# Kernel optimization log

Measured on AMD Instinct MI355X. Metric: run time of the kernel, lower is better.

## Reference

```python
import jax, jax.numpy as jnp
import numpy as np

B, N, P_FEATS = 8, 4096, 3
WIDTH, HEADS, LAYERS, N_LAT = 768, 12, 8, 256
NUM_FREQS = 8
D_HEAD = WIDTH // HEADS
SCALE = 1.0 / np.sqrt(np.sqrt(D_HEAD))  # applied to q and k separately
IN_DIM = 3 * (1 + 2 * NUM_FREQS) + P_FEATS  # 54
EPS = 1e-5


def fourier_embed(pc):
    # pc: [B,N,3] -> [B,N,51] (include_input + sin/cos at freqs 2^0..2^7)
    freqs = (2.0 ** jnp.arange(NUM_FREQS)).astype(pc.dtype)
    ang = pc[..., None] * freqs  # [B,N,3,F]
    ang = ang.reshape(*pc.shape[:-1], 3 * NUM_FREQS)
    return jnp.concatenate([pc, jnp.sin(ang), jnp.cos(ang)], axis=-1)


def layernorm(x, s, b):
    mu = jnp.mean(x, axis=-1, keepdims=True)
    var = jnp.mean(jnp.square(x - mu), axis=-1, keepdims=True)
    return (x - mu) * jax.lax.rsqrt(var + EPS) * s + b


def mh_attn(q, k, v):
    # q: [B,T,H,C], k/v: [B,S,H,C]
    w = jnp.einsum('bthc,bshc->bhts', q * SCALE, k * SCALE)
    w = jax.nn.softmax(w.astype(jnp.float32), axis=-1).astype(q.dtype)
    out = jnp.einsum('bhts,bshc->bthc', w, v)
    return out.reshape(*q.shape[:2], -1)


def setup_inputs() -> dict:
    key = jax.random.key(0)
    ks = iter(jax.random.split(key, 64))
    rn = lambda shape, std=0.02: jax.random.normal(next(ks), shape, jnp.float32) * std
    inp = {
        'pc': jax.random.normal(next(ks), (B, N, 3), jnp.float32),
        'feats': jax.random.uniform(next(ks), (B, N, P_FEATS), jnp.float32),
        'query': rn((N_LAT, WIDTH)),
        'in_W': rn((WIDTH, IN_DIM)), 'in_b': jnp.zeros((WIDTH,)),
        'ca_qkv_W': rn((3 * WIDTH, WIDTH)), 'ca_qkv_b': jnp.zeros((3 * WIDTH,)),
        'ca_proj_W': rn((WIDTH, WIDTH)), 'ca_proj_b': jnp.zeros((WIDTH,)),
        'ln1_s': jnp.ones((LAYERS, WIDTH)), 'ln1_b': jnp.zeros((LAYERS, WIDTH)),
        'qkv_W': rn((LAYERS, 3 * WIDTH, WIDTH)), 'qkv_b': jnp.zeros((LAYERS, 3 * WIDTH)),
        'proj_W': rn((LAYERS, WIDTH, WIDTH)), 'proj_b': jnp.zeros((LAYERS, WIDTH)),
        'ln2_s': jnp.ones((LAYERS, WIDTH)), 'ln2_b': jnp.zeros((LAYERS, WIDTH)),
        'fc_W': rn((LAYERS, 4 * WIDTH, WIDTH)), 'fc_b': jnp.zeros((LAYERS, 4 * WIDTH)),
        'fc2_W': rn((LAYERS, WIDTH, 4 * WIDTH)), 'fc2_b': jnp.zeros((LAYERS, WIDTH)),
    }
    return inp


def _forward(pc, feats, query, in_W, in_b, ca_qkv_W, ca_qkv_b, ca_proj_W, ca_proj_b,
             ln1_s, ln1_b, qkv_W, qkv_b, proj_W, proj_b, ln2_s, ln2_b,
             fc_W, fc_b, fc2_W, fc2_b):
    bs = pc.shape[0]
    data = jnp.concatenate([fourier_embed(pc), feats], axis=-1)  # [B,N,54]
    data = data @ in_W.T + in_b  # [B,N,W]
    q_lat = jnp.broadcast_to(query[None], (bs, N_LAT, WIDTH))

    # --- cross attention (no residual, matching source) ---
    q = (q_lat @ ca_qkv_W.T + ca_qkv_b)[..., :WIDTH]
    kv = data @ ca_qkv_W.T + ca_qkv_b
    k, v = kv[..., WIDTH:2 * WIDTH], kv[..., 2 * WIDTH:]
    q = q.reshape(bs, N_LAT, HEADS, D_HEAD)
    k = k.reshape(bs, N, HEADS, D_HEAD)
    v = v.reshape(bs, N, HEADS, D_HEAD)
    latents = mh_attn(q, k, v) @ ca_proj_W.T + ca_proj_b  # [B,L,W]

    # --- self-attention transformer stack via scan ---
    def block(x, p):
        (l1s, l1b, qW, qb, pW, pb, l2s, l2b, fW, fb, f2W, f2b) = p
        h = layernorm(x, l1s, l1b)
        qkv = (h @ qW.T + qb).reshape(bs, N_LAT, HEADS, 3 * D_HEAD)
        qh, kh, vh = jnp.split(qkv, 3, axis=-1)
        x = x + mh_attn(qh, kh, vh) @ pW.T + pb
        h = layernorm(x, l2s, l2b)
        h = jax.nn.gelu(h @ fW.T + fb, approximate=False) @ f2W.T + f2b
        return x + h, None

    params = (ln1_s, ln1_b, qkv_W, qkv_b, proj_W, proj_b, ln2_s, ln2_b, fc_W, fc_b, fc2_W, fc2_b)
    latents, _ = jax.lax.scan(block, latents, params)
    return latents, pc


def reference(pc, feats, query, in_W, in_b, ca_qkv_W, ca_qkv_b, ca_proj_W, ca_proj_b,
              ln1_s, ln1_b, qkv_W, qkv_b, proj_W, proj_b, ln2_s, ln2_b,
              fc_W, fc_b, fc2_W, fc2_b):
    return _forward(pc, feats, query, in_W, in_b, ca_qkv_W, ca_qkv_b, ca_proj_W, ca_proj_b,
                    ln1_s, ln1_b, qkv_W, qkv_b, proj_W, proj_b, ln2_s, ln2_b,
                    fc_W, fc_b, fc2_W, fc2_b)
```

## Files before the change

### kernel.cpp

```cpp
#include <hip/hip_runtime.h>
#include <stdint.h>

typedef unsigned short u16;
typedef __bf16 bf16x8 __attribute__((ext_vector_type(8)));
typedef float f32x4 __attribute__((ext_vector_type(4)));

#define DEVINL __device__ __forceinline__

DEVINL u16 f2bf(float f) {
  union { float f; unsigned u; } c; c.f = f;
  unsigned u = c.u + 0x7FFFu + ((c.u >> 16) & 1u);
  return (u16)(u >> 16);
}

DEVINL float bf2f(u16 v) {
  union { unsigned u; float f; } c; c.u = (unsigned)v << 16;
  return c.f;
}

DEVINL unsigned pk2bf(float a, float b) {
#if __has_builtin(__builtin_amdgcn_cvt_pk_bf16_f32)
  auto r = __builtin_amdgcn_cvt_pk_bf16_f32(a, b);
  unsigned u;
  __builtin_memcpy(&u, &r, 4);
  return u;
#else
  return (unsigned)f2bf(a) | ((unsigned)f2bf(b) << 16);
#endif
}

DEVINL void gl2lds16(const void* g, void* l) {
  __builtin_amdgcn_global_load_lds(
      (const __attribute__((address_space(1))) unsigned int*)g,
      (__attribute__((address_space(3))) unsigned int*)l, 16, 0, 0);
}

template <int N> DEVINL void waitvm() {
  asm volatile("s_waitcnt vmcnt(%0)" ::"n"(N) : "memory");
}
DEVINL void bar() {
  asm volatile("" ::: "memory");
  __builtin_amdgcn_s_barrier();
  asm volatile("" ::: "memory");
}

__global__ __launch_bounds__(256) void cvt4_kernel(
    const float* __restrict__ s0, u16* __restrict__ d0, int n0,
    const float* __restrict__ s1, u16* __restrict__ d1, int n1,
    const float* __restrict__ s2, u16* __restrict__ d2, int n2,
    const float* __restrict__ s3, u16* __restrict__ d3, int n3) {
  int i = blockIdx.x * 256 + threadIdx.x;
  const float* s; u16* d;
  if (i < n0) { s = s0; d = d0; }
  else {
    i -= n0;
    if (i < n1) { s = s1; d = d1; }
    else {
      i -= n1;
      if (i < n2) { s = s2; d = d2; }
      else {
        i -= n2;
        if (i >= n3) return;
        s = s3; d = d3;
      }
    }
  }
  float4 v = ((const float4*)s)[i];
  ((uint2*)d)[i] = make_uint2(pk2bf(v.x, v.y), pk2bf(v.z, v.w));
}

__global__ __launch_bounds__(256) void pad_inwT_kernel(const float* __restrict__ src,
                                                       u16* __restrict__ dst) {
  int t = blockIdx.x * 256 + threadIdx.x;
  if (t >= 64 * 768) return;
  int j = t / 768, o = t - j * 768;
  dst[t] = (j < 54) ? f2bf(src[o * 54 + j]) : (u16)0;
}

__global__ __launch_bounds__(256) void bprime_kernel(const float* __restrict__ caW,
                                                     const float* __restrict__ caB,
                                                     const float* __restrict__ inb,
                                                     float* __restrict__ bp) {
  int w = threadIdx.x >> 6, lane = threadIdx.x & 63;
  int m = blockIdx.x * 4 + w;
  const float* row = caW + (size_t)(768 + m) * 768;
  float s = 0.f;
#pragma unroll
  for (int k = 0; k < 12; k++) s += row[lane + k * 64] * inb[lane + k * 64];
#pragma unroll
  for (int msk = 32; msk >= 1; msk >>= 1) s += __shfl_xor(s, msk, 64);
  if (lane == 0) bp[m] = s + caB[768 + m];
}

__global__ __launch_bounds__(256) void embed_kernel(const float* __restrict__ pc,
                                                    const float* __restrict__ feats,
                                                    u16* __restrict__ emb) {
  int t = blockIdx.x * 256 + threadIdx.x;
  int p = t >> 6, c = t & 63;
  float v = 0.f;
  if (c < 3) {
    v = pc[p * 3 + c];
  } else if (c < 27) {
    int i = c - 3;
    float f = (float)(1 << (i & 7));
    v = sinf(pc[p * 3 + (i >> 3)] * f);
  } else if (c < 51) {
    int i = c - 27;
    float f = (float)(1 << (i & 7));
    v = cosf(pc[p * 3 + (i >> 3)] * f);
  } else if (c < 54) {
    v = feats[p * 3 + (c - 51)];
  }
  emb[t] = f2bf(v);
}

template <int TM, int TN, int WR, int WC, int MODE>
__global__ __launch_bounds__(256) void gemm_t(
    const u16* __restrict__ A, const u16* __restrict__ Bw,
    const float* __restrict__ bias, const float* __restrict__ resid,
    float* __restrict__ outF, u16* __restrict__ outB,
    int M, int N, int Nout, int K, int gelu,
    u16* __restrict__ vt, int vy, int skvt, int bsh) {
  constexpr int IM = TM / WR / 16;
  constexpr int IN = TN / WC / 16;
  __shared__ u16 As[TM * 32];
  __shared__ u16 Bs[TN * 32];
  const int tid = threadIdx.x;
  const int lane = tid & 63, w = tid >> 6;
  const int l15 = lane & 15, quad = lane >> 4;
  const int mblk = blockIdx.x * TM, nblk = blockIdx.y * TN;
  const int wm = (w % WR) * (TM / WR);
  const int wn = (w / WR) * (TN / WC);

  f32x4 acc[IM][IN];
#pragma unroll
  for (int i = 0; i < IM; i++)
#pragma unroll
    for (int j = 0; j < IN; j++) acc[i][j] = f32x4{0.f, 0.f, 0.f, 0.f};

  bool tv = false;
  if (MODE == 1) tv = ((int)blockIdx.y >= vy);
  if (MODE == 2) tv = ((int)(blockIdx.y % 3) == 2);

  if (!tv) {
    for (int k0 = 0; k0 < K; k0 += 32) {
#pragma unroll
      for (int s = tid; s < TM * 4; s += 256) {
        int row = s >> 2, c8 = (s & 3) << 3;
        gl2lds16(A + (size_t)(mblk + row) * K + (k0 + c8), &As[s * 8]);
      }
#pragma unroll
      for (int s = tid; s < TN * 4; s += 256) {
        int row = s >> 2, c8 = (s & 3) << 3;
        gl2lds16(Bw + (size_t)(nblk + row) * K + (k0 + c8), &Bs[s * 8]);
      }
      __syncthreads();
      bf16x8 af[IM], bfr[IN];
#pragma unroll
      for (int i = 0; i < IM; i++)
        af[i] = *(const bf16x8*)&As[(wm + i * 16 + l15) * 32 + quad * 8];
#pragma unroll
      for (int j = 0; j < IN; j++)
        bfr[j] = *(const bf16x8*)&Bs[(wn + j * 16 + l15) * 32 + quad * 8];
#pragma unroll
      for (int i = 0; i < IM; i++)
#pragma unroll
        for (int j = 0; j < IN; j++)
          acc[i][j] = __builtin_amdgcn_mfma_f32_16x16x32_bf16(bfr[j], af[i], acc[i][j], 0, 0, 0);
      __syncthreads();
    }
#pragma unroll
    for (int i = 0; i < IM; i++) {
      int m = mblk + wm + i * 16 + l15;
#pragma unroll
      for (int j = 0; j < IN; j++) {
        int n0 = nblk + wn + j * 16 + quad * 4;
        float4 bv = bias ? *(const float4*)&bias[n0] : make_float4(0.f, 0.f, 0.f, 0.f);
        float v0 = acc[i][j][0] + bv.x;
        float v1 = acc[i][j][1] + bv.y;
        float v2 = acc[i][j][2] + bv.z;
        float v3 = acc[i][j][3] + bv.w;
        if (gelu) {
          v0 = 0.5f * v0 * (1.0f + erff(v0 * 0.70710678118f));
          v1 = 0.5f * v1 * (1.0f + erff(v1 * 0.70710678118f));
          v2 = 0.5f * v2 * (1.0f + erff(v2 * 0.70710678118f));
          v3 = 0.5f * v3 * (1.0f + erff(v3 * 0.70710678118f));
        }
        size_t idx = (size_t)m * Nout + n0;
        if (resid) {
          float4 rv = *(const float4*)&resid[idx];
          v0 += rv.x; v1 += rv.y; v2 += rv.z; v3 += rv.w;
        }
        if (outF) {
          float4 ov = {v0, v1, v2, v3};
          *(float4*)&outF[idx] = ov;
        }
        if (outB) {
          *(uint2*)&outB[idx] = make_uint2(pk2bf(v0, v1), pk2bf(v2, v3));
        }
      }
    }
  } else {
    for (int k0 = 0; k0 < K; k0 += 32) {
#pragma unroll
      for (int s = tid; s < TM * 4; s += 256) {
        int row = s >> 2, c8 = (s & 3) << 3;
        gl2lds16(A + (size_t)(mblk + row) * K + (k0 + c8), &As[s * 8]);
      }
#pragma unroll
      for (int s = tid; s < TN * 4; s += 256) {
        int row = s >> 2, c8 = (s & 3) << 3;
        gl2lds16(Bw + (size_t)(nblk + row) * K + (k0 + c8), &Bs[s * 8]);
      }
      __syncthreads();
      bf16x8 af[IM], bfr[IN];
#pragma unroll
      for (int i = 0; i < IM; i++)
        af[i] = *(const bf16x8*)&As[(wm + i * 16 + l15) * 32 + quad * 8];
#pragma unroll
      for (int j = 0; j < IN; j++)
        bfr[j] = *(const bf16x8*)&Bs[(wn + j * 16 + l15) * 32 + quad * 8];
#pragma unroll
      for (int i = 0; i < IM; i++)
#pragma unroll
        for (int j = 0; j < IN; j++)
          acc[i][j] = __builtin_amdgcn_mfma_f32_16x16x32_bf16(af[i], bfr[j], acc[i][j], 0, 0, 0);
      __syncthreads();
    }
    int msk = (1 << bsh) - 1;
#pragma unroll
    for (int j = 0; j < IN; j++) {
      int n = nblk + wn + j * 16 + l15;
      float bv = bias ? bias[n] : 0.f;
#pragma unroll
      for (int i = 0; i < IM; i++) {
        int m0 = mblk + wm + i * 16 + quad * 4;
        int b = m0 >> bsh;
        int s0 = m0 & msk;
        float v0 = acc[i][j][0] + bv;
        float v1 = acc[i][j][1] + bv;
        float v2 = acc[i][j][2] + bv;
        float v3 = acc[i][j][3] + bv;
        size_t vrow;
        if (MODE == 2) {
          int h = blockIdx.y / 3;
          vrow = (size_t)(b * 12 + h) * 64 + (wn + j * 16 + l15);
        } else {
          vrow = (size_t)b * 768 + (n - vy * TN);
        }
        size_t addr = vrow * skvt + s0;
        *(uint2*)&vt[addr] = make_uint2(pk2bf(v0, v1), pk2bf(v2, v3));
      }
    }
  }
}

template <int TM, int TN, int WR, int WC>
__global__ __launch_bounds__(256) void gemmsk_t(
    const u16* __restrict__ A, const u16* __restrict__ Bw,
    float* __restrict__ P, int M, int N, int K, int kchunk) {
  constexpr int IM = TM / WR / 16;
  constexpr int IN = TN / WC / 16;
  __shared__ u16 As[TM * 32];
  __shared__ u16 Bs[TN * 32];
  const int tid = threadIdx.x;
  const int lane = tid & 63, w = tid >> 6;
  const int l15 = lane & 15, quad = lane >> 4;
  const int mblk = blockIdx.x * TM, nblk = blockIdx.y * TN;
  const int wm = (w % WR) * (TM / WR);
  const int wn = (w / WR) * (TN / WC);
  const int kbeg = blockIdx.z * kchunk;
  const int kend = kbeg + kchunk;

  f32x4 acc[IM][IN];
#pragma unroll
  for (int i = 0; i < IM; i++)
#pragma unroll
    for (int j = 0; j < IN; j++) acc[i][j] = f32x4{0.f, 0.f, 0.f, 0.f};

  for (int k0 = kbeg; k0 < kend; k0 += 32) {
#pragma unroll
    for (int s = tid; s < TM * 4; s += 256) {
      int row = s >> 2, c8 = (s & 3) << 3;
      gl2lds16(A + (size_t)(mblk + row) * K + (k0 + c8), &As[s * 8]);
    }
#pragma unroll
    for (int s = tid; s < TN * 4; s += 256) {
      int row = s >> 2, c8 = (s & 3) << 3;
      gl2lds16(Bw + (size_t)(nblk + row) * K + (k0 + c8), &Bs[s * 8]);
    }
    __syncthreads();
    bf16x8 af[IM], bfr[IN];
#pragma unroll
    for (int i = 0; i < IM; i++)
      af[i] = *(const bf16x8*)&As[(wm + i * 16 + l15) * 32 + quad * 8];
#pragma unroll
    for (int j = 0; j < IN; j++)
      bfr[j] = *(const bf16x8*)&Bs[(wn + j * 16 + l15) * 32 + quad * 8];
#pragma unroll
    for (int i = 0; i < IM; i++)
#pragma unroll
      for (int j = 0; j < IN; j++)
        acc[i][j] = __builtin_amdgcn_mfma_f32_16x16x32_bf16(bfr[j], af[i], acc[i][j], 0, 0, 0);
    __syncthreads();
  }

  float* Pz = P + (size_t)blockIdx.z * M * N;
#pragma unroll
  for (int i = 0; i < IM; i++) {
    int m = mblk + wm + i * 16 + l15;
#pragma unroll
    for (int j = 0; j < IN; j++) {
      int n0 = nblk + wn + j * 16 + quad * 4;
      float4 ov = {acc[i][j][0], acc[i][j][1], acc[i][j][2], acc[i][j][3]};
      *(float4*)&Pz[(size_t)m * N + n0] = ov;
    }
  }
}

__global__ __launch_bounds__(256) void skred_kernel(
    const float* __restrict__ P, int nsk, int MN4, int N,
    const float* __restrict__ bias, const float* __restrict__ resid,
    float* __restrict__ outF, u16* __restrict__ outB) {
  int i = blockIdx.x * 256 + threadIdx.x;
  if (i >= MN4) return;
  float4 s = ((const float4*)P)[i];
  for (int z = 1; z < nsk; z++) {
    float4 t = ((const float4*)P)[(size_t)z * MN4 + i];
    s.x += t.x; s.y += t.y; s.z += t.z; s.w += t.w;
  }
  if (bias) {
    int n0 = (i * 4) % N;
    float4 b = *(const float4*)&bias[n0];
    s.x += b.x; s.y += b.y; s.z += b.z; s.w += b.w;
  }
  if (resid) {
    float4 r = ((const float4*)resid)[i];
    s.x += r.x; s.y += r.y; s.z += r.z; s.w += r.w;
  }
  if (outF) ((float4*)outF)[i] = s;
  if (outB) ((uint2*)outB)[i] = make_uint2(pk2bf(s.x, s.y), pk2bf(s.z, s.w));
}

__global__ __launch_bounds__(256) void flash_kernel(
    const u16* __restrict__ Q, long qb, int qrs, int qhs,
    const u16* __restrict__ Kp, long kb, int krs, int khs,
    const u16* __restrict__ Vt, u16* __restrict__ Out,
    u16* __restrict__ Part, float* __restrict__ Ml,
    int Skv, int nsplit, int kvlen, int nbh, float scale2) {
  __shared__ u16 Qs[64 * 64];
  __shared__ u16 Ks[2][64 * 64];
  __shared__ u16 Vs[2][64 * 64];
  __shared__ u16 Ps[64 * 72];

  const int tid = threadIdx.x;
  const int lane = tid & 63, w = tid >> 6;
  const int l15 = lane & 15, quad = lane >> 4;

  int bid = blockIdx.x;
  int grp = nbh * nsplit;
  int qt = bid / grp;
  int rem = bid - qt * grp;
  int bh = rem / nsplit;
  int split = rem - bh * nsplit;
  int h = bh % 12, b = bh / 12;

  const u16* Qbase = Q + (size_t)b * qb + (size_t)(qt * 64) * qrs + h * qhs;
  const u16* Kbase = Kp + (size_t)b * kb + (size_t)h * khs;
  const u16* Vbase = Vt + ((size_t)(b * 12 + h) * 64) * Skv;

  int kt0 = split * kvlen;

#pragma unroll
  for (int p = 0; p < 2; ++p) {
    int slot = tid + p * 256;
    int row = slot >> 3, c = slot & 7;
    int cg = (c - row) & 7;
    gl2lds16(Qbase + (size_t)row * qrs + cg * 8, &Qs[slot * 8]);
    gl2lds16(Kbase + (size_t)(kt0 + row) * krs + cg * 8, &Ks[0][slot * 8]);
    gl2lds16(Vbase + (size_t)row * Skv + kt0 + cg * 8, &Vs[0][slot * 8]);
  }
  __syncthreads();

  bf16x8 qa[2];
#pragma unroll
  for (int kk = 0; kk < 2; kk++)
    qa[kk] = *(const bf16x8*)&Qs[(w * 16 + l15) * 64 + ((kk * 4 + quad + l15) & 7) * 8];

  f32x4 zero = {0.f, 0.f, 0.f, 0.f};
  f32x4 O[4];
#pragma unroll
  for (int d = 0; d < 4; d++) O[d] = zero;
  float m_i = -1e30f, l_i = 0.f;

  int cur = 0;
  for (int kt = kt0; kt < kt0 + kvlen; kt += 64) {
    bool hasnext = (kt + 64 < kt0 + kvlen);
    if (hasnext) {
#pragma unroll
      for (int p = 0; p < 2; ++p) {
        int slot = tid + p * 256;
        int row = slot >> 3, c = slot & 7;
        int cg = (c - row) & 7;
        gl2lds16(Kbase + (size_t)(kt + 64 + row) * krs + cg * 8, &Ks[cur ^ 1][slot * 8]);
        gl2lds16(Vbase + (size_t)row * Skv + (kt + 64) + cg * 8, &Vs[cur ^ 1][slot * 8]);
      }
      waitvm<4>();
    } else {
      waitvm<0>();
    }
    bar();

    f32x4 St[4];
#pragma unroll
    for (int j = 0; j < 4; j++) St[j] = zero;
#pragma unroll
    for (int kk = 0; kk < 2; kk++) {
#pragma unroll
      for (int j = 0; j < 4; j++) {
        bf16x8 kf = *(const bf16x8*)&Ks[cur][(j * 16 + l15) * 64 + ((kk * 4 + quad + l15) & 7) * 8];
        St[j] = __builtin_amdgcn_mfma_f32_16x16x32_bf16(kf, qa[kk], St[j], 0, 0, 0);
      }
    }

    float mx = St[0][0];
#pragma unroll
    for (int j = 0; j < 4; j++)
#pragma unroll
      for (int r = 0; r < 4; r++) mx = fmaxf(mx, St[j][r]);
    mx = fmaxf(mx, __shfl_xor(mx, 16, 64));
    mx = fmaxf(mx, __shfl_xor(mx, 32, 64));
    mx *= scale2;

    bool skip = __all(mx <= m_i + 8.f);
    float al = 1.f;
    if (!skip) {
      float mnew = fmaxf(m_i, mx);
      al = __expf(m_i - mnew);
      m_i = mnew;
    }
    float mref = m_i;
    float sum = 0.f;
#pragma unroll
    for (int j = 0; j < 4; j++) {
      float p0 = __expf(fmaf(St[j][0], scale2, -mref));
      float p1 = __expf(fmaf(St[j][1], scale2, -mref));
      float p2 = __expf(fmaf(St[j][2], scale2, -mref));
      float p3 = __expf(fmaf(St[j][3], scale2, -mref));
      sum += (p0 + p1) + (p2 + p3);
      *(uint2*)&Ps[(w * 16 + l15) * 72 + j * 16 + quad * 4] =
          make_uint2(pk2bf(p0, p1), pk2bf(p2, p3));
    }
    sum += __shfl_xor(sum, 16, 64);
    sum += __shfl_xor(sum, 32, 64);

    if (skip) {
      l_i += sum;
    } else {
      l_i = l_i * al + sum;
      float a0 = __shfl(al, quad * 20 + 0, 64);
      float a1 = __shfl(al, quad * 20 + 1, 64);
      float a2 = __shfl(al, quad * 20 + 2, 64);
      float a3 = __shfl(al, quad * 20 + 3, 64);
#pragma unroll
      for (int d = 0; d < 4; d++) {
        O[d][0] *= a0; O[d][1] *= a1; O[d][2] *= a2; O[d][3] *= a3;
      }
    }
    __asm__ __volatile__("s_waitcnt lgkmcnt(0)" ::: "memory");
#pragma unroll
    for (int kk = 0; kk < 2; kk++) {
      bf16x8 pa = *(const bf16x8*)&Ps[(w * 16 + l15) * 72 + kk * 32 + quad * 8];
#pragma unroll
      for (int d = 0; d < 4; d++) {
        bf16x8 vf = *(const bf16x8*)&Vs[cur][(d * 16 + l15) * 64 + ((kk * 4 + quad + l15) & 7) * 8];
        O[d] = __builtin_amdgcn_mfma_f32_16x16x32_bf16(pa, vf, O[d], 0, 0, 0);
      }
    }
    bar();
    cur ^= 1;
  }

  float l0 = __shfl(l_i, quad * 20 + 0, 64);
  float l1 = __shfl(l_i, quad * 20 + 1, 64);
  float l2 = __shfl(l_i, quad * 20 + 2, 64);
  float l3 = __shfl(l_i, quad * 20 + 3, 64);

  if (nsplit == 1) {
    float inv0 = 1.f / l0, inv1 = 1.f / l1, inv2 = 1.f / l2, inv3 = 1.f / l3;
    u16* Ob = Out + ((size_t)(b * 256 + qt * 64 + w * 16 + quad * 4)) * 768 + h * 64 + l15;
#pragma unroll
    for (int d = 0; d < 4; d++) {
      Ob[(size_t)0 * 768 + d * 16] = f2bf(O[d][0] * inv0);
      Ob[(size_t)1 * 768 + d * 16] = f2bf(O[d][1] * inv1);
      Ob[(size_t)2 * 768 + d * 16] = f2bf(O[d][2] * inv2);
      Ob[(size_t)3 * 768 + d * 16] = f2bf(O[d][3] * inv3);
    }
  } else {
    float m0 = __shfl(m_i, quad * 20 + 0, 64);
    float m1 = __shfl(m_i, quad * 20 + 1, 64);
    float m2 = __shfl(m_i, quad * 20 + 2, 64);
    float m3 = __shfl(m_i, quad * 20 + 3, 64);
    u16* Pb = Part + ((size_t)(bh * 4 + qt) * nsplit + split) * 4096;
    int rowb = w * 16 + quad * 4;
#pragma unroll
    for (int d = 0; d < 4; d++) {
      Pb[(rowb + 0) * 64 + d * 16 + l15] = f2bf(O[d][0]);
      Pb[(rowb + 1) * 64 + d * 16 + l15] = f2bf(O[d][1]);
      Pb[(rowb + 2) * 64 + d * 16 + l15] = f2bf(O[d][2]);
      Pb[(rowb + 3) * 64 + d * 16 + l15] = f2bf(O[d][3]);
    }
    if (l15 == 0) {
      float* MlB = Ml + ((size_t)(bh * 4 + qt) * nsplit + split) * 128;
      MlB[rowb + 0] = m0; MlB[rowb + 1] = m1; MlB[rowb + 2] = m2; MlB[rowb + 3] = m3;
      MlB[64 + rowb + 0] = l0; MlB[64 + rowb + 1] = l1;
      MlB[64 + rowb + 2] = l2; MlB[64 + rowb + 3] = l3;
    }
  }
}

__global__ __launch_bounds__(256) void freduce_kernel(
    const u16* __restrict__ Part, const float* __restrict__ Ml,
    u16* __restrict__ Out, int nsplit) {
  int bid = blockIdx.x;
  int qt = bid & 3, bh = bid >> 2;
  int h = bh % 12, b = bh / 12;
  int tid = threadIdx.x;
  int r = tid >> 2, dc = tid & 3;
  const float* mlb = Ml + (size_t)(bh * 4 + qt) * nsplit * 128;
  float M = -1e30f;
  for (int s = 0; s < nsplit; s++) M = fmaxf(M, mlb[s * 128 + r]);
  float L = 0.f;
  float accv[16];
#pragma unroll
  for (int i = 0; i < 16; i++) accv[i] = 0.f;
  const u16* pb = Part + (size_t)(bh * 4 + qt) * nsplit * 4096 + r * 64 + dc * 16;
  for (int s = 0; s < nsplit; s++) {
    float wgt = __expf(mlb[s * 128 + r] - M);
    L += wgt * mlb[s * 128 + 64 + r];
    u16 tmp[16];
    *(uint4*)tmp = *(const uint4*)(pb + s * 4096);
    *(uint4*)(tmp + 8) = *(const uint4*)(pb + s * 4096 + 8);
#pragma unroll
    for (int i = 0; i < 16; i++) accv[i] += wgt * bf2f(tmp[i]);
  }
  float inv = 1.f / L;
  unsigned ot[8];
#pragma unroll
  for (int i = 0; i < 8; i++)
    ot[i] = pk2bf(accv[2 * i] * inv, accv[2 * i + 1] * inv);
  u16* ob = Out + ((size_t)(b * 256 + qt * 64 + r)) * 768 + h * 64 + dc * 16;
  *(uint4*)ob = *(uint4*)ot;
  *(uint4*)(ob + 8) = *(uint4*)(ot + 4);
}

__global__ __launch_bounds__(256) void ln_kernel(const float* __restrict__ X,
                                                 const float* __restrict__ sc,
                                                 const float* __restrict__ bi,
                                                 u16* __restrict__ Hout) {
  int row = blockIdx.x;
  int tid = threadIdx.x;
  const float* x = X + (size_t)row * 768;
  float v0 = x[tid], v1 = x[tid + 256], v2 = x[tid + 512];
  float s = v0 + v1 + v2;
  float q = v0 * v0 + v1 * v1 + v2 * v2;
#pragma unroll
  for (int m = 1; m < 64; m <<= 1) {
    s += __shfl_xor(s, m, 64);
    q += __shfl_xor(q, m, 64);
  }
  __shared__ float rs[4], rq[4];
  if ((tid & 63) == 0) { rs[tid >> 6] = s; rq[tid >> 6] = q; }
  __syncthreads();
  s = rs[0] + rs[1] + rs[2] + rs[3];
  q = rq[0] + rq[1] + rq[2] + rq[3];
  float mu = s * (1.f / 768.f);
  float var = q * (1.f / 768.f) - mu * mu;
  float rstd = rsqrtf(var + 1e-5f);
  u16* ho = Hout + (size_t)row * 768;
  ho[tid]       = f2bf((v0 - mu) * rstd * sc[tid]       + bi[tid]);
  ho[tid + 256] = f2bf((v1 - mu) * rstd * sc[tid + 256] + bi[tid + 256]);
  ho[tid + 512] = f2bf((v2 - mu) * rstd * sc[tid + 512] + bi[tid + 512]);
}

__global__ __launch_bounds__(256) void copy4_kernel(const float* __restrict__ src,
                                                    float* __restrict__ dst, int n4) {
  int i = blockIdx.x * 256 + threadIdx.x;
  if (i < n4) ((float4*)dst)[i] = ((const float4*)src)[i];
}

extern "C" void kernel_launch(void* const* d_in, const int* in_sizes, int n_in,
                              void* d_out, int out_size, void* d_ws, size_t ws_size,
                              hipStream_t stream) {
  const float* pc        = (const float*)d_in[0];
  const float* feats     = (const float*)d_in[1];
  const float* query     = (const float*)d_in[2];
  const float* in_W      = (const float*)d_in[3];
  const float* in_b      = (const float*)d_in[4];
  const float* ca_qkv_W  = (const float*)d_in[5];
  const float* ca_qkv_b  = (const float*)d_in[6];
  const float* ca_proj_W = (const float*)d_in[7];
  const float* ca_proj_b = (const float*)d_in[8];
  const float* ln1_s     = (const float*)d_in[9];
  const float* ln1_b     = (const float*)d_in[10];
  const float* qkv_W     = (const float*)d_in[11];
  const float* qkv_b     = (const float*)d_in[12];
  const float* proj_W    = (const float*)d_in[13];
  const float* proj_b    = (const float*)d_in[14];
  const float* ln2_s     = (const float*)d_in[15];
  const float* ln2_b     = (const float*)d_in[16];
  const float* fc_W      = (const float*)d_in[17];
  const float* fc_b      = (const float*)d_in[18];
  const float* fc2_W     = (const float*)d_in[19];
  const float* fc2_b     = (const float*)d_in[20];

  char* base = (char*)d_ws;
  size_t off = 0;
  auto alloc = [&](size_t bytes) -> char* {
    char* p = base + off;
    off += (bytes + 255) & ~(size_t)255;
    return p;
  };

  u16* WqT     = (u16*)alloc(64 * 768 * 2);
  u16* Wquery  = (u16*)alloc(256 * 768 * 2);
  u16* Wcaqkv  = (u16*)alloc(2304 * 768 * 2);
  u16* Wcaproj = (u16*)alloc(768 * 768 * 2);
  u16* Wkp     = (u16*)alloc(1536 * 64 * 2);
  float* bprime = (float*)alloc(1536 * 4);
  u16* qc      = (u16*)alloc(256 * 768 * 2);
  u16* attn    = (u16*)alloc((size_t)2048 * 768 * 2);
  u16* hbuf    = (u16*)alloc((size_t)2048 * 768 * 2);
  char* uni    = alloc(13369344);
  u16* qkvb    = (u16*)uni;
  u16* VtS     = (u16*)(uni + 9437184);
  u16* fc1     = (u16*)uni;
  u16* Part    = (u16*)uni;
  float* Ml    = (float*)(uni + 12582912);

  size_t fixed_end = off;
  const size_t wAllSz = (size_t)8 * (2304 * 768 + 768 * 768 + 2 * 3072 * 768) * 2;
  auto crossSz = [](int cb) {
    return (size_t)cb * 4096 * 64 * 2 + 2 * ((size_t)cb * 4096 * 768 * 2);
  };

  bool allw; int CB;
  if (fixed_end + (wAllSz > crossSz(8) ? wAllSz : crossSz(8)) + 65536 <= ws_size) {
    allw = true;  CB = 8;
  } else if (fixed_end + 14155776 + crossSz(2) + 65536 <= ws_size) {
    allw = false; CB = 2;
  } else {
    allw = false; CB = 1;
  }

  u16 *WqkvB, *WprojB, *WfcB, *Wfc2B, *emb, *kvbK, *VtC;
  if (allw) {
    char* X = base + off;
    WqkvB  = (u16*)X;
    WprojB = WqkvB + (size_t)8 * 2304 * 768;
    WfcB   = WprojB + (size_t)8 * 768 * 768;
    Wfc2B  = WfcB + (size_t)8 * 3072 * 768;
    emb  = (u16*)X;
    kvbK = (u16*)(X + (size_t)CB * 4096 * 64 * 2);
    VtC  = (u16*)(X + (size_t)CB * 4096 * 64 * 2 + (size_t)CB * 4096 * 768 * 2);
    off = fixed_end + (wAllSz > crossSz(8) ? wAllSz : crossSz(8));
  } else {
    WqkvB  = (u16*)alloc(2304 * 768 * 2);
    WprojB = (u16*)alloc(768 * 768 * 2);
    WfcB   = (u16*)alloc(3072 * 768 * 2);
    Wfc2B  = (u16*)alloc((size_t)768 * 3072 * 2);
    emb  = (u16*)alloc((size_t)CB * 4096 * 64 * 2);
    kvbK = (u16*)alloc((size_t)CB * 4096 * 768 * 2);
    VtC  = (u16*)alloc((size_t)CB * 4096 * 768 * 2);
  }

  const size_t pb2048 = (size_t)2048 * 768 * 4;
  auto fits = [&](size_t bytes) { return off + bytes + 4096 <= ws_size; };
  int nsk_fc2 = fits(4 * pb2048) ? 4 : (fits(2 * pb2048) ? 2 : 1);
  int nsk_pr  = fits(2 * pb2048) ? 2 : 1;
  int nsk_qc  = fits((size_t)256 * 768 * 4 * 8) ? 8 : 1;
  float* skP  = (float*)(base + off);

  float* latents = (float*)d_out;
  const float scale2 = 0.125f;

  {
    int n0 = 256 * 768 / 4, n1 = 2304 * 768 / 4, n2 = 768 * 768 / 4;
    cvt4_kernel<<<(n0 + n1 + n2 + 255) / 256, 256, 0, stream>>>(
        query, Wquery, n0, ca_qkv_W, Wcaqkv, n1, ca_proj_W, Wcaproj, n2,
        nullptr, nullptr, 0);
  }
  pad_inwT_kernel<<<192, 256, 0, stream>>>(in_W, WqT);
  gemm_t<64, 64, 2, 2, 0><<<dim3(24, 1), 256, 0, stream>>>(
      Wcaqkv + (size_t)768 * 768, WqT, nullptr, nullptr, nullptr, Wkp,
      1536, 64, 64, 768, 0, nullptr, 0, 0, 0);
  bprime_kernel<<<384, 256, 0, stream>>>(ca_qkv_W, ca_qkv_b, in_b, bprime);

  if (nsk_qc > 1) {
    gemmsk_t<64, 64, 2, 2><<<dim3(4, 12, nsk_qc), 256, 0, stream>>>(
        Wquery, Wcaqkv, skP, 256, 768, 768, 768 / nsk_qc);
    skred_kernel<<<192, 256, 0, stream>>>(
        skP, nsk_qc, 256 * 768 / 4, 768, ca_qkv_b, nullptr, nullptr, qc);
  } else {
    gemm_t<64, 64, 2, 2, 0><<<dim3(4, 12), 256, 0, stream>>>(
        Wquery, Wcaqkv, ca_qkv_b, nullptr, nullptr, qc,
        256, 768, 768, 768, 0, nullptr, 0, 0, 0);
  }

  int nchunk = 8 / CB;
  for (int c = 0; c < nchunk; ++c) {
    int Mc = CB * 4096;
    const float* pc_c = pc + (size_t)c * Mc * 3;
    const float* ft_c = feats + (size_t)c * Mc * 3;
    embed_kernel<<<Mc / 4, 256, 0, stream>>>(pc_c, ft_c, emb);
    gemm_t<128, 128, 2, 2, 1><<<dim3(Mc / 128, 12), 256, 0, stream>>>(
        emb, Wkp, bprime, nullptr, nullptr, kvbK,
        Mc, 1536, 768, 64, 0, VtC, 6, 4096, 12);
    flash_kernel<<<CB * 12 * 16, 256, 0, stream>>>(
        qc, 0L, 768, 64, kvbK, (long)4096 * 768, 768, 64, VtC,
        nullptr, Part, Ml, 4096, 4, 1024, CB * 12, scale2);
    freduce_kernel<<<CB * 48, 256, 0, stream>>>(
        Part, Ml, attn + (size_t)c * CB * 256 * 768, 4);
  }
  if (nsk_pr > 1) {
    gemmsk_t<64, 64, 2, 2><<<dim3(32, 12, nsk_pr), 256, 0, stream>>>(
        attn, Wcaproj, skP, 2048, 768, 768, 768 / nsk_pr);
    skred_kernel<<<1536, 256, 0, stream>>>(
        skP, nsk_pr, 2048 * 768 / 4, 768, ca_proj_b, nullptr, latents, nullptr);
  } else {
    gemm_t<64, 64, 2, 2, 0><<<dim3(32, 12), 256, 0, stream>>>(
        attn, Wcaproj, ca_proj_b, nullptr, latents, nullptr,
        2048, 768, 768, 768, 0, nullptr, 0, 0, 0);
  }

  if (allw) {
    int n0 = 8 * 2304 * 768 / 4, n1 = 8 * 768 * 768 / 4, n2 = 8 * 3072 * 768 / 4;
    cvt4_kernel<<<(n0 + n1 + 2 * n2 + 255) / 256, 256, 0, stream>>>(
        qkv_W, WqkvB, n0, proj_W, WprojB, n1, fc_W, WfcB, n2, fc2_W, Wfc2B, n2);
  }

  for (int l = 0; l < 8; ++l) {
    u16* Wlq  = allw ? WqkvB  + (size_t)l * 2304 * 768 : WqkvB;
    u16* Wlp  = allw ? WprojB + (size_t)l * 768 * 768  : WprojB;
    u16* Wlf  = allw ? WfcB   + (size_t)l * 3072 * 768 : WfcB;
    u16* Wlf2 = allw ? Wfc2B  + (size_t)l * 3072 * 768 : Wfc2B;
    if (!allw) {
      int n0 = 2304 * 768 / 4, n1 = 768 * 768 / 4, n2 = 3072 * 768 / 4;
      cvt4_kernel<<<(n0 + n1 + 2 * n2 + 255) / 256, 256, 0, stream>>>(
          qkv_W + (size_t)l * 2304 * 768, Wlq, n0,
          proj_W + (size_t)l * 768 * 768, Wlp, n1,
          fc_W + (size_t)l * 3072 * 768, Wlf, n2,
          fc2_W + (size_t)l * 768 * 3072, Wlf2, n2);
    }
    ln_kernel<<<2048, 256, 0, stream>>>(latents, ln1_s + l * 768, ln1_b + l * 768, hbuf);
    gemm_t<64, 64, 2, 2, 2><<<dim3(32, 36), 256, 0, stream>>>(
        hbuf, Wlq, qkv_b + l * 2304, nullptr, nullptr, qkvb,
        2048, 2304, 2304, 768, 0, VtS, 0, 256, 8);
    flash_kernel<<<384, 256, 0, stream>>>(
        qkvb, (long)256 * 2304, 2304, 192, qkvb + 64, (long)256 * 2304, 2304, 192,
        VtS, attn, nullptr, nullptr, 256, 1, 256, 96, scale2);
    if (nsk_pr > 1) {
      gemmsk_t<64, 64, 2, 2><<<dim3(32, 12, nsk_pr), 256, 0, stream>>>(
          attn, Wlp, skP, 2048, 768, 768, 768 / nsk_pr);
      skred_kernel<<<1536, 256, 0, stream>>>(
          skP, nsk_pr, 2048 * 768 / 4, 768, proj_b + l * 768, latents, latents, nullptr);
    } else {
      gemm_t<64, 64, 2, 2, 0><<<dim3(32, 12), 256, 0, stream>>>(
          attn, Wlp, proj_b + l * 768, latents, latents, nullptr,
          2048, 768, 768, 768, 0, nullptr, 0, 0, 0);
    }
    ln_kernel<<<2048, 256, 0, stream>>>(latents, ln2_s + l * 768, ln2_b + l * 768, hbuf);
    gemm_t<64, 128, 1, 4, 0><<<dim3(32, 24), 256, 0, stream>>>(
        hbuf, Wlf, fc_b + l * 3072, nullptr, nullptr, fc1,
        2048, 3072, 3072, 768, 1, nullptr, 0, 0, 0);
    if (nsk_fc2 > 1) {
      gemmsk_t<64, 64, 2, 2><<<dim3(32, 12, nsk_fc2), 256, 0, stream>>>(
          fc1, Wlf2, skP, 2048, 768, 3072, 3072 / nsk_fc2);
      skred_kernel<<<1536, 256, 0, stream>>>(
          skP, nsk_fc2, 2048 * 768 / 4, 768, fc2_b + l * 768, latents, latents, nullptr);
    } else {
      gemm_t<64, 64, 2, 2, 0><<<dim3(32, 12), 256, 0, stream>>>(
          fc1, Wlf2, fc2_b + l * 768, latents, latents, nullptr,
          2048, 768, 768, 3072, 0, nullptr, 0, 0, 0);
    }
  }

  copy4_kernel<<<96, 256, 0, stream>>>(pc, (float*)d_out + (size_t)2048 * 768, 98304 / 4);
}
```

Measured before the change: 1.293 ms.

## Single-buffer flash attention LDS with register prefetch and aliased Q/P tiles

Replaces the double-buffered K/V tiles loaded directly into LDS with a single LDS buffer. The next tile is prefetched into registers during compute and written to LDS between barriers. The Q tile and P scratch share one region, roughly halving LDS use per block so more blocks fit on each CU. The cost is extra VGPRs for the staged tiles, an additional barrier per iteration, and the loss of the asynchronous direct-to-LDS load path.

```diff
diff --git a/kernel.cpp b/kernel.cpp
--- a/kernel.cpp
+++ b/kernel.cpp
@@ -35,9 +35,7 @@
       (__attribute__((address_space(3))) unsigned int*)l, 16, 0, 0);
 }
 
-template <int N> DEVINL void waitvm() {
-  asm volatile("s_waitcnt vmcnt(%0)" ::"n"(N) : "memory");
-}
+DEVINL void waitlgkm0() { asm volatile("s_waitcnt lgkmcnt(0)" ::: "memory"); }
 DEVINL void bar() {
   asm volatile("" ::: "memory");
   __builtin_amdgcn_s_barrier();
@@ -348,10 +346,11 @@
     const u16* __restrict__ Vt, u16* __restrict__ Out,
     u16* __restrict__ Part, float* __restrict__ Ml,
     int Skv, int nsplit, int kvlen, int nbh, float scale2) {
-  __shared__ u16 Qs[64 * 64];
-  __shared__ u16 Ks[2][64 * 64];
-  __shared__ u16 Vs[2][64 * 64];
-  __shared__ u16 Ps[64 * 72];
+  __shared__ u16 SH[64 * 72 + 2 * 64 * 64];
+  u16* const Qs = SH;
+  u16* const Ps = SH;
+  u16* const Ks = SH + 64 * 72;
+  u16* const Vs = SH + 64 * 72 + 64 * 64;
 
   const int tid = threadIdx.x;
   const int lane = tid & 63, w = tid >> 6;
@@ -377,8 +376,8 @@
     int row = slot >> 3, c = slot & 7;
     int cg = (c - row) & 7;
     gl2lds16(Qbase + (size_t)row * qrs + cg * 8, &Qs[slot * 8]);
-    gl2lds16(Kbase + (size_t)(kt0 + row) * krs + cg * 8, &Ks[0][slot * 8]);
-    gl2lds16(Vbase + (size_t)row * Skv + kt0 + cg * 8, &Vs[0][slot * 8]);
+    gl2lds16(Kbase + (size_t)(kt0 + row) * krs + cg * 8, &Ks[slot * 8]);
+    gl2lds16(Vbase + (size_t)row * Skv + kt0 + cg * 8, &Vs[slot * 8]);
   }
   __syncthreads();
 
@@ -386,6 +385,8 @@
 #pragma unroll
   for (int kk = 0; kk < 2; kk++)
     qa[kk] = *(const bf16x8*)&Qs[(w * 16 + l15) * 64 + ((kk * 4 + quad + l15) & 7) * 8];
+  waitlgkm0();
+  bar();
 
   f32x4 zero = {0.f, 0.f, 0.f, 0.f};
   f32x4 O[4];
@@ -393,23 +394,18 @@
   for (int d = 0; d < 4; d++) O[d] = zero;
   float m_i = -1e30f, l_i = 0.f;
 
-  int cur = 0;
+  const int srow = tid >> 3;
+  const int scg = ((tid & 7) - srow) & 7;
+
   for (int kt = kt0; kt < kt0 + kvlen; kt += 64) {
     bool hasnext = (kt + 64 < kt0 + kvlen);
+    uint4 kreg0, kreg1, vreg0, vreg1;
     if (hasnext) {
-#pragma unroll
-      for (int p = 0; p < 2; ++p) {
-        int slot = tid + p * 256;
-        int row = slot >> 3, c = slot & 7;
-        int cg = (c - row) & 7;
-        gl2lds16(Kbase + (size_t)(kt + 64 + row) * krs + cg * 8, &Ks[cur ^ 1][slot * 8]);
-        gl2lds16(Vbase + (size_t)row * Skv + (kt + 64) + cg * 8, &Vs[cur ^ 1][slot * 8]);
-      }
-      waitvm<4>();
-    } else {
-      waitvm<0>();
-    }
-    bar();
+      kreg0 = *(const uint4*)(Kbase + (size_t)(kt + 64 + srow) * krs + scg * 8);
+      kreg1 = *(const uint4*)(Kbase + (size_t)(kt + 64 + srow + 32) * krs + scg * 8);
+      vreg0 = *(const uint4*)(Vbase + (size_t)srow * Skv + (kt + 64) + scg * 8);
+      vreg1 = *(const uint4*)(Vbase + (size_t)(srow + 32) * Skv + (kt + 64) + scg * 8);
+    }
 
     f32x4 St[4];
 #pragma unroll
@@ -418,7 +414,7 @@
     for (int kk = 0; kk < 2; kk++) {
 #pragma unroll
       for (int j = 0; j < 4; j++) {
-        bf16x8 kf = *(const bf16x8*)&Ks[cur][(j * 16 + l15) * 64 + ((kk * 4 + quad + l15) & 7) * 8];
+        bf16x8 kf = *(const bf16x8*)&Ks[(j * 16 + l15) * 64 + ((kk * 4 + quad + l15) & 7) * 8];
         St[j] = __builtin_amdgcn_mfma_f32_16x16x32_bf16(kf, qa[kk], St[j], 0, 0, 0);
       }
     }
@@ -467,18 +463,26 @@
         O[d][0] *= a0; O[d][1] *= a1; O[d][2] *= a2; O[d][3] *= a3;
       }
     }
-    __asm__ __volatile__("s_waitcnt lgkmcnt(0)" ::: "memory");
+    waitlgkm0();
 #pragma unroll
     for (int kk = 0; kk < 2; kk++) {
       bf16x8 pa = *(const bf16x8*)&Ps[(w * 16 + l15) * 72 + kk * 32 + quad * 8];
 #pragma unroll
       for (int d = 0; d < 4; d++) {
-        bf16x8 vf = *(const bf16x8*)&Vs[cur][(d * 16 + l15) * 64 + ((kk * 4 + quad + l15) & 7) * 8];
+        bf16x8 vf = *(const bf16x8*)&Vs[(d * 16 + l15) * 64 + ((kk * 4 + quad + l15) & 7) * 8];
         O[d] = __builtin_amdgcn_mfma_f32_16x16x32_bf16(pa, vf, O[d], 0, 0, 0);
       }
     }
-    bar();
-    cur ^= 1;
+
+    if (hasnext) {
+      bar();
+      *(uint4*)&Ks[tid * 8] = kreg0;
+      *(uint4*)&Ks[(tid + 256) * 8] = kreg1;
+      *(uint4*)&Vs[tid * 8] = vreg0;
+      *(uint4*)&Vs[(tid + 256) * 8] = vreg1;
+      waitlgkm0();
+      bar();
+    }
   }
 
   float l0 = __shfl(l_i, quad * 20 + 0, 64);
```

Result: no change. 1.302 ms (+0.7%).
